# Optimization experiments

Hardware: AMD Instinct MI355X
Metric: run time of the kernel (lower is better)

Reference implementation:

```python
import jax, jax.numpy as jnp
import numpy as np
import math

B, T, D = 2, 2048, 2048
N_HEADS, N_KV, HEAD_DIM = 16, 4, 128
INTER = 8192
MAX_POS = 4096
ROPE_BASE = 10000.0
EPS = 1e-6


def _rope_tables():
    inv_freq = 1.0 / (ROPE_BASE ** (jnp.arange(0, HEAD_DIM, 2, dtype=jnp.float32) / HEAD_DIM))
    t = jnp.arange(MAX_POS, dtype=jnp.float32)
    freqs = jnp.einsum('i,j->ij', t, inv_freq)          # [MAX_POS, HEAD_DIM//2]
    emb = jnp.concatenate([freqs, freqs], axis=-1)      # [MAX_POS, HEAD_DIM]
    return jnp.cos(emb), jnp.sin(emb)


def _apply_rope(x, cos, sin):
    # x: [B,H,T,Dh]; cos/sin: [B,T,Dh] (gathered by position_ids)
    c = cos[:, None, :, :]
    s = sin[:, None, :, :]
    x1 = x[..., ::2]
    x2 = x[..., 1::2]
    x_rot = jnp.stack([-x2, x1], axis=-1).reshape(x.shape)  # interleave(-x2, x1)
    return x * c + x_rot * s


def _rms_norm(x, w):
    var = jnp.mean(x * x, axis=-1, keepdims=True)
    return w * (x * jax.lax.rsqrt(var + EPS))


def setup_inputs() -> dict:
    key = jax.random.key(0)
    ks = jax.random.split(key, 10)
    s = 0.02
    hidden_states = jax.random.normal(ks[0], (B, T, D), dtype=jnp.float32)
    # additive causal mask
    causal = jnp.tril(jnp.ones((T, T), dtype=bool))
    attention_mask = jnp.where(causal, 0.0, -1e9).astype(jnp.float32)[None, None]
    position_ids = jnp.arange(B * T).reshape(B, T)  # values < MAX_POS
    return {
        'hidden_states': hidden_states,
        'attention_mask': attention_mask,
        'position_ids': position_ids,
        'attn_norm_w': jnp.ones((D,), jnp.float32),
        'mlp_norm_w': jnp.ones((D,), jnp.float32),
        'wq': jax.random.normal(ks[1], (D, N_HEADS * HEAD_DIM), jnp.float32) * s,
        'wk': jax.random.normal(ks[2], (D, N_KV * HEAD_DIM), jnp.float32) * s,
        'wv': jax.random.normal(ks[3], (D, N_KV * HEAD_DIM), jnp.float32) * s,
        'wo': jax.random.normal(ks[4], (N_HEADS * HEAD_DIM, D), jnp.float32) * s,
        'gate_w': jax.random.normal(ks[5], (D, D), jnp.float32) * s,
        'gate_b': jnp.zeros((D,), jnp.float32),
        'fc1_w': jax.random.normal(ks[6], (D, INTER), jnp.float32) * s,
        'fc2_w': jax.random.normal(ks[7], (INTER, D), jnp.float32) * s,
    }


def reference(hidden_states, attention_mask, position_ids, attn_norm_w, mlp_norm_w,
              wq, wk, wv, wo, gate_w, gate_b, fc1_w, fc2_w):
    b, t, _ = hidden_states.shape
    residual = hidden_states
    h = _rms_norm(hidden_states, attn_norm_w)

    # elementwise sigmoid output gate: [B,T,D] -> [B,H,T,Dh]
    gate = jax.nn.sigmoid(h @ gate_w + gate_b)
    gate = gate.reshape(b, t, N_HEADS, HEAD_DIM).transpose(0, 2, 1, 3)

    q = (h @ wq).reshape(b, t, N_HEADS, HEAD_DIM).transpose(0, 2, 1, 3)
    k = (h @ wk).reshape(b, t, N_KV, HEAD_DIM).transpose(0, 2, 1, 3)
    v = (h @ wv).reshape(b, t, N_KV, HEAD_DIM).transpose(0, 2, 1, 3)

    cos_t, sin_t = _rope_tables()
    cos = cos_t[position_ids]  # [B,T,Dh]
    sin = sin_t[position_ids]
    q = _apply_rope(q, cos, sin)
    k = _apply_rope(k, cos, sin)

    n_rep = N_HEADS // N_KV
    k = jnp.repeat(k, n_rep, axis=1)  # GQA expand to [B,H,T,Dh]
    v = jnp.repeat(v, n_rep, axis=1)

    scores = jnp.einsum('bhqd,bhkd->bhqk', q, k) / math.sqrt(HEAD_DIM)
    scores = scores + attention_mask
    attn = jax.nn.softmax(scores, axis=-1)
    out = jnp.einsum('bhqk,bhkd->bhqd', attn, v) * gate
    out = out.transpose(0, 2, 1, 3).reshape(b, t, N_HEADS * HEAD_DIM) @ wo

    h = residual + out
    residual = h
    h2 = _rms_norm(h, mlp_norm_w)
    mlp_out = jax.nn.silu(h2 @ fc1_w) @ fc2_w
    return residual + mlp_out
```

## Files before the change

### kernel.cpp

```cpp
#include <hip/hip_runtime.h>
#include <hip/hip_bf16.h>
#include <cstdint>
#include <cstddef>

#define BB 2
#define TT 2048
#define DD 2048
#define NH 16
#define NKV 4
#define HD 128
#define NI 8192
#define MM (BB*TT)

typedef __bf16 bf16x8 __attribute__((ext_vector_type(8)));
typedef float  f32x4  __attribute__((ext_vector_type(4)));

__device__ __forceinline__ void gload_lds16(const void* g, void* l) {
  __builtin_amdgcn_global_load_lds((__attribute__((address_space(1))) void*)g,
                                   (__attribute__((address_space(3))) void*)l,
                                   16, 0, 0);
}

__device__ __forceinline__ int xcd_swizzle(int wg, int nwg) {
  int xcd = wg & 7;
  int l = wg >> 3;
  int q = nwg >> 3, r = nwg & 7;
  return (xcd < r ? xcd * (q + 1) : r * (q + 1) + (xcd - r) * q) + l;
}

__global__ __launch_bounds__(128) void rope_tables_k(float* __restrict__ cosT,
                                                     float* __restrict__ sinT) {
  int pos = blockIdx.x;
  int d = threadIdx.x;
  int f = d & 63;
  float inv = powf(10000.0f, -((float)(2 * f)) / 128.0f);
  float ang = inv * (float)pos;
  cosT[pos * 128 + d] = cosf(ang);
  sinT[pos * 128 + d] = sinf(ang);
}

template <typename TIN>
__global__ __launch_bounds__(256) void transpose_to_bf16_k(const TIN* __restrict__ in,
                                                           __bf16* __restrict__ out,
                                                           int R, int C) {
  __shared__ float t[32][33];
  int c0 = blockIdx.x * 32, r0 = blockIdx.y * 32;
  int tx = threadIdx.x & 31;
  int ty = threadIdx.x >> 5;
#pragma unroll
  for (int i = 0; i < 4; i++) {
    int r = ty + i * 8;
    t[r][tx] = (float)in[(size_t)(r0 + r) * C + c0 + tx];
  }
  __syncthreads();
#pragma unroll
  for (int i = 0; i < 4; i++) {
    int r = ty + i * 8;
    out[(size_t)(c0 + r) * R + r0 + tx] = (__bf16)t[tx][r];
  }
}

__global__ __launch_bounds__(256) void rmsnorm_k(const float* __restrict__ x,
                                                 const float* __restrict__ w,
                                                 __bf16* __restrict__ out) {
  int row = blockIdx.x;
  const float* xr = x + (size_t)row * DD;
  int t = threadIdx.x;
  float4 a = ((const float4*)xr)[2 * t];
  float4 b = ((const float4*)xr)[2 * t + 1];
  float ss = a.x * a.x + a.y * a.y + a.z * a.z + a.w * a.w +
             b.x * b.x + b.y * b.y + b.z * b.z + b.w * b.w;
#pragma unroll
  for (int off = 32; off; off >>= 1) ss += __shfl_xor(ss, off, 64);
  __shared__ float red[4];
  if ((t & 63) == 0) red[t >> 6] = ss;
  __syncthreads();
  float tot = red[0] + red[1] + red[2] + red[3];
  float rs = rsqrtf(tot * (1.0f / DD) + 1e-6f);
  const float4 w1 = ((const float4*)w)[2 * t];
  const float4 w2 = ((const float4*)w)[2 * t + 1];
  bf16x8 ov;
  ov[0] = (__bf16)(a.x * rs * w1.x);
  ov[1] = (__bf16)(a.y * rs * w1.y);
  ov[2] = (__bf16)(a.z * rs * w1.z);
  ov[3] = (__bf16)(a.w * rs * w1.w);
  ov[4] = (__bf16)(b.x * rs * w2.x);
  ov[5] = (__bf16)(b.y * rs * w2.y);
  ov[6] = (__bf16)(b.z * rs * w2.z);
  ov[7] = (__bf16)(b.w * rs * w2.w);
  *(bf16x8*)(out + (size_t)row * DD + t * 8) = ov;
}

enum { G_QG = 0, G_RES = 1, G_SILU = 2, G_PART = 3 };

template <int EPI>
__global__ __launch_bounds__(512) void gemm256_k(
    const __bf16* __restrict__ A, const __bf16* __restrict__ Bt,
    __bf16* __restrict__ outB, float* __restrict__ outF,
    __bf16* __restrict__ outQ, __bf16* __restrict__ outG,
    const float* __restrict__ bias, const float* __restrict__ residual,
    const float* __restrict__ cosT, const float* __restrict__ sinT,
    const int* __restrict__ posids, int N, int K, int ldk, float oscale) {
  __shared__ __align__(16) __bf16 Ab[3][256 * 32];
  __shared__ __align__(16) __bf16 Bb[3][256 * 32];
  const int tid = threadIdx.x;
  const int lane = tid & 63;
  const int wid = tid >> 6;
  const int wr = wid >> 2;
  const int wc = wid & 3;
  const int fr = lane & 15;
  const int fg = lane >> 4;

  const int nwg = gridDim.x * gridDim.y;
  int wg = xcd_swizzle(blockIdx.y * gridDim.x + blockIdx.x, nwg);
  const int bx = wg % gridDim.x, by = wg / gridDim.x;
  const int m0 = by * 256;
  const int n0 = bx * 256;
  const int kz = blockIdx.z;
  const int kBase = kz * K;

  const int srow0 = wid * 32 + (lane >> 2);
  const int scol = (((lane & 3) ^ ((lane >> 3) & 3)) << 3);
  const __bf16* aS0 = A + (size_t)(m0 + srow0) * ldk + kBase + scol;
  const __bf16* aS1 = aS0 + (size_t)16 * ldk;
  const __bf16* bS0 = Bt + (size_t)(n0 + srow0) * ldk + kBase + scol;
  const __bf16* bS1 = bS0 + (size_t)16 * ldk;
  const int e0 = (wid * 2) * 512;
  const int e1 = (wid * 2 + 1) * 512;

  const int nt = K / 32;

#define STAGE_A(kt, s)                          \
  {                                             \
    const int k0_ = (kt) * 32;                  \
    gload_lds16(aS0 + k0_, &Ab[(s)][e0]);       \
    gload_lds16(aS1 + k0_, &Ab[(s)][e1]);       \
  }
#define STAGE_B(kt, s)                          \
  {                                             \
    const int k0_ = (kt) * 32;                  \
    gload_lds16(bS0 + k0_, &Bb[(s)][e0]);       \
    gload_lds16(bS1 + k0_, &Bb[(s)][e1]);       \
  }

  STAGE_A(0, 0);
  STAGE_B(0, 0);
  STAGE_A(1, 1);
  STAGE_B(1, 1);
  asm volatile("s_waitcnt vmcnt(4)" ::: "memory");
  __builtin_amdgcn_s_barrier();

  f32x4 acc[8][4];
#pragma unroll
  for (int i = 0; i < 8; i++)
#pragma unroll
    for (int j = 0; j < 4; j++) acc[i][j] = (f32x4){0.f, 0.f, 0.f, 0.f};

  const int asl = (fg ^ ((fr >> 1) & 3)) * 8;

  for (int t = 0; t < nt; ++t) {
    const int s = t % 3;
    const int sn = (t + 2) % 3;
    bf16x8 af[4], bfr[4];
#pragma unroll
    for (int mi = 0; mi < 4; mi++)
      af[mi] = *(const bf16x8*)&Ab[s][(wr * 128 + mi * 16 + fr) * 32 + asl];
#pragma unroll
    for (int ni = 0; ni < 4; ni++)
      bfr[ni] = *(const bf16x8*)&Bb[s][(wc * 64 + ni * 16 + fr) * 32 + asl];
    if (t + 2 < nt) STAGE_A(t + 2, sn);
    __builtin_amdgcn_s_barrier();
    asm volatile("s_waitcnt lgkmcnt(0)" ::: "memory");
    __builtin_amdgcn_sched_barrier(0);
    __builtin_amdgcn_s_setprio(1);
#pragma unroll
    for (int mi = 0; mi < 4; mi++)
#pragma unroll
      for (int ni = 0; ni < 4; ni++)
        acc[mi][ni] =
            __builtin_amdgcn_mfma_f32_16x16x32_bf16(af[mi], bfr[ni], acc[mi][ni], 0, 0, 0);
    __builtin_amdgcn_s_setprio(0);
    __builtin_amdgcn_s_barrier();
    bf16x8 af2[4];
#pragma unroll
    for (int mi = 0; mi < 4; mi++)
      af2[mi] = *(const bf16x8*)&Ab[s][(wr * 128 + (mi + 4) * 16 + fr) * 32 + asl];
    if (t + 2 < nt) {
      STAGE_B(t + 2, sn);
      asm volatile("s_waitcnt vmcnt(4)" ::: "memory");
    } else {
      asm volatile("s_waitcnt vmcnt(0)" ::: "memory");
    }
    __builtin_amdgcn_s_barrier();
    asm volatile("s_waitcnt lgkmcnt(0)" ::: "memory");
    __builtin_amdgcn_sched_barrier(0);
    __builtin_amdgcn_s_setprio(1);
#pragma unroll
    for (int mi = 0; mi < 4; mi++)
#pragma unroll
      for (int ni = 0; ni < 4; ni++)
        acc[mi + 4][ni] =
            __builtin_amdgcn_mfma_f32_16x16x32_bf16(af2[mi], bfr[ni], acc[mi + 4][ni], 0, 0, 0);
    __builtin_amdgcn_s_setprio(0);
    __builtin_amdgcn_s_barrier();
  }
#undef STAGE_A
#undef STAGE_B

#pragma unroll
  for (int mi = 0; mi < 8; mi++) {
    const int row = m0 + wr * 128 + mi * 16 + fg * 4;
#pragma unroll
    for (int ni = 0; ni < 4; ni++) {
      const int col = n0 + wc * 64 + ni * 16 + fr;
#pragma unroll
      for (int j = 0; j < 4; j++) {
        float v = acc[mi][ni][j];
        const int r = row + j;
        if constexpr (EPI == G_QG) {
          float vp = __shfl_xor(v, 1, 64);
          if (n0 < 2048) {
            int pos = posids[r];
            int d = col & 127;
            float c = cosT[pos * 128 + d], sn2 = sinT[pos * 128 + d];
            float o = (col & 1) ? (v * c + vp * sn2) : (v * c - vp * sn2);
            outQ[(size_t)r * 2048 + col] = (__bf16)(o * oscale);
          } else {
            float xx = v + bias[col - 2048];
            outG[(size_t)r * 2048 + (col - 2048)] = (__bf16)(1.0f / (1.0f + expf(-xx)));
          }
        } else if constexpr (EPI == G_RES) {
          outF[(size_t)r * N + col] = v + residual[(size_t)r * N + col];
        } else if constexpr (EPI == G_SILU) {
          outB[(size_t)r * N + col] = (__bf16)(v / (1.0f + expf(-v)));
        } else {
          outB[(size_t)(kz * MM + r) * N + col] = (__bf16)v;
        }
      }
    }
  }
}

__global__ __launch_bounds__(256) void combine_k(const __bf16* __restrict__ parts,
                                                 const float* __restrict__ res,
                                                 float* __restrict__ out) {
  size_t i = ((size_t)blockIdx.x * 256 + threadIdx.x) * 8;
  bf16x8 p0 = *(const bf16x8*)&parts[i];
  bf16x8 p1 = *(const bf16x8*)&parts[(size_t)MM * 2048 + i];
  float4 a = *(const float4*)&res[i];
  float4 b = *(const float4*)&res[i + 4];
  float4 o0, o1;
  o0.x = (float)p0[0] + (float)p1[0] + a.x;
  o0.y = (float)p0[1] + (float)p1[1] + a.y;
  o0.z = (float)p0[2] + (float)p1[2] + a.z;
  o0.w = (float)p0[3] + (float)p1[3] + a.w;
  o1.x = (float)p0[4] + (float)p1[4] + b.x;
  o1.y = (float)p0[5] + (float)p1[5] + b.y;
  o1.z = (float)p0[6] + (float)p1[6] + b.z;
  o1.w = (float)p0[7] + (float)p1[7] + b.w;
  *(float4*)&out[i] = o0;
  *(float4*)&out[i + 4] = o1;
}

__global__ __launch_bounds__(256) void gemm_kv_k(
    const __bf16* __restrict__ A, const __bf16* __restrict__ Bt,
    __bf16* __restrict__ kOut, __bf16* __restrict__ vOut,
    const float* __restrict__ cosT, const float* __restrict__ sinT,
    const int* __restrict__ posids, int K) {
  __shared__ __align__(16) __bf16 As[128 * 32];
  __shared__ __align__(16) __bf16 Bs[128 * 32];
  const int tid = threadIdx.x;
  const int lane = tid & 63;
  const int w = tid >> 6;
  const int wm = w >> 1, wn = w & 1;

  const int nwg = gridDim.x * gridDim.y;
  int wg = xcd_swizzle(blockIdx.y * gridDim.x + blockIdx.x, nwg);
  const int bx = wg % gridDim.x, by = wg / gridDim.x;
  const int m0 = by * 128;
  const int n0 = bx * 128;

  const int lr = lane >> 2;
  const int lc = (lane & 3) * 8;
  const __bf16* aSrc = A + (size_t)(m0 + 32 * w + lr) * K + lc;
  const __bf16* bSrc = Bt + (size_t)(n0 + 32 * w + lr) * K + lc;
  __bf16* aDst = &As[w * 1024];
  __bf16* bDst = &Bs[w * 1024];

  f32x4 acc[4][4];
#pragma unroll
  for (int i = 0; i < 4; i++)
#pragma unroll
    for (int j = 0; j < 4; j++) acc[i][j] = (f32x4){0.f, 0.f, 0.f, 0.f};

  const int fr = lane & 15;
  const int fc = (lane >> 4) * 8;

  for (int k0 = 0; k0 < K; k0 += 32) {
    __syncthreads();
    gload_lds16(aSrc + k0, aDst);
    gload_lds16(aSrc + k0 + (size_t)16 * K, aDst + 512);
    gload_lds16(bSrc + k0, bDst);
    gload_lds16(bSrc + k0 + (size_t)16 * K, bDst + 512);
    asm volatile("s_waitcnt vmcnt(0)" ::: "memory");
    __syncthreads();

    bf16x8 af[4], bfg[4];
#pragma unroll
    for (int i = 0; i < 4; i++)
      af[i] = *(const bf16x8*)&As[(wm * 64 + i * 16 + fr) * 32 + fc];
#pragma unroll
    for (int i = 0; i < 4; i++)
      bfg[i] = *(const bf16x8*)&Bs[(wn * 64 + i * 16 + fr) * 32 + fc];
#pragma unroll
    for (int mi = 0; mi < 4; mi++)
#pragma unroll
      for (int ni = 0; ni < 4; ni++)
        acc[mi][ni] =
            __builtin_amdgcn_mfma_f32_16x16x32_bf16(af[mi], bfg[ni], acc[mi][ni], 0, 0, 0);
  }

  const int fg = lane >> 4;
#pragma unroll
  for (int mi = 0; mi < 4; mi++) {
#pragma unroll
    for (int ni = 0; ni < 4; ni++) {
#pragma unroll
      for (int j = 0; j < 4; j++) {
        int row = m0 + wm * 64 + mi * 16 + fg * 4 + j;
        int col = n0 + wn * 64 + ni * 16 + fr;
        float v = acc[mi][ni][j];
        float vp = __shfl_xor(v, 1, 64);
        if (col < 512) {
          int pos = posids[row];
          int d = col & 127;
          float c = cosT[pos * 128 + d];
          float s = sinT[pos * 128 + d];
          float o = (col & 1) ? (v * c + vp * s) : (v * c - vp * s);
          kOut[(size_t)row * 512 + col] = (__bf16)o;
        } else {
          vOut[(size_t)row * 512 + (col - 512)] = (__bf16)v;
        }
      }
    }
  }
}

__global__ __launch_bounds__(256) void attn_k(const __bf16* __restrict__ Q,
                                              const __bf16* __restrict__ Kb,
                                              const __bf16* __restrict__ Vt,
                                              const __bf16* __restrict__ Gate,
                                              __bf16* __restrict__ Out) {
  __shared__ __align__(16) __bf16 Ks[2][64 * 128];
  __shared__ __align__(16) __bf16 Vs[2][128 * 64];
  __shared__ __align__(16) __bf16 Ps[4][16 * 64];
  const int tid = threadIdx.x;
  const int lane = tid & 63;
  const int w = tid >> 6;
  const int fr = lane & 15;
  const int fg = lane >> 4;

  const int nwg = gridDim.x * gridDim.y;
  int wg = xcd_swizzle(blockIdx.y * gridDim.x + blockIdx.x, nwg);
  const int qb = wg % gridDim.x;
  const int bh = wg / gridDim.x;
  const int q0 = qb * 64;
  const int b = bh >> 4, h = bh & 15;
  const int g = h >> 2;

  const size_t qrow = (size_t)(b * TT + q0 + w * 16 + fr);
  bf16x8 qf[4];
#pragma unroll
  for (int kt = 0; kt < 4; kt++)
    qf[kt] = *(const bf16x8*)&Q[qrow * 2048 + h * 128 + kt * 32 + fg * 8];

  const __bf16* kPtr[4];
  const __bf16* vPtr[4];
#pragma unroll
  for (int i = 0; i < 4; i++) {
    int krow = w * 16 + i * 4 + (lane >> 4);
    int kcol8 = (lane & 15) ^ (krow & 15);
    kPtr[i] = Kb + (size_t)(b * TT + krow) * 512 + g * 128 + kcol8 * 8;
    int dloc = w * 32 + i * 8 + (lane >> 3);
    int kv8 = (lane & 7) ^ (dloc & 7);
    vPtr[i] = Vt + (size_t)(g * 128 + dloc) * (size_t)MM + b * TT + kv8 * 8;
  }

  f32x4 o[8];
#pragma unroll
  for (int i = 0; i < 8; i++) o[i] = (f32x4){0.f, 0.f, 0.f, 0.f};
  float mrow[4] = {-3e38f, -3e38f, -3e38f, -3e38f};
  float lrow[4] = {0.f, 0.f, 0.f, 0.f};

  const int nsteps = qb + 1;

#pragma unroll
  for (int i = 0; i < 4; i++) {
    gload_lds16(kPtr[i], &Ks[0][w * 2048 + i * 512]);
    gload_lds16(vPtr[i], &Vs[0][w * 2048 + i * 512]);
  }
  __syncthreads();

  for (int t = 0; t < nsteps; t++) {
    const int cur = t & 1;
    const int kb = t * 64;
    if (t + 1 < nsteps) {
      const int nb = kb + 64;
#pragma unroll
      for (int i = 0; i < 4; i++) {
        gload_lds16(kPtr[i] + (size_t)nb * 512, &Ks[cur ^ 1][w * 2048 + i * 512]);
        gload_lds16(vPtr[i] + nb, &Vs[cur ^ 1][w * 2048 + i * 512]);
      }
    }

    f32x4 s[4];
#pragma unroll
    for (int nc = 0; nc < 4; nc++) s[nc] = (f32x4){0.f, 0.f, 0.f, 0.f};
#pragma unroll
    for (int nc = 0; nc < 4; nc++)
#pragma unroll
      for (int kt = 0; kt < 4; kt++) {
        bf16x8 kf = *(const bf16x8*)&Ks[cur][(nc * 16 + fr) * 128 + (((kt * 4 + fg) ^ fr) << 3)];
        s[nc] = __builtin_amdgcn_mfma_f32_16x16x32_bf16(qf[kt], kf, s[nc], 0, 0, 0);
      }

    float alpha[4];
#pragma unroll
    for (int j = 0; j < 4; j++) {
      const int qr = q0 + w * 16 + fg * 4 + j;
      float pv[4];
#pragma unroll
      for (int nc = 0; nc < 4; nc++) {
        int kc = kb + nc * 16 + fr;
        float val = s[nc][j];
        if (kc > qr) val = -1e9f;
        pv[nc] = val;
      }
      float tmx = fmaxf(fmaxf(pv[0], pv[1]), fmaxf(pv[2], pv[3]));
      tmx = fmaxf(tmx, __shfl_xor(tmx, 1, 64));
      tmx = fmaxf(tmx, __shfl_xor(tmx, 2, 64));
      tmx = fmaxf(tmx, __shfl_xor(tmx, 4, 64));
      tmx = fmaxf(tmx, __shfl_xor(tmx, 8, 64));
      float mnew = fmaxf(mrow[j], tmx);
      alpha[j] = __expf(mrow[j] - mnew);
      mrow[j] = mnew;
      float rsum = 0.f;
      const int q = fg * 4 + j;
#pragma unroll
      for (int nc = 0; nc < 4; nc++) {
        float e = __expf(pv[nc] - mnew);
        rsum += e;
        Ps[w][q * 64 + (((nc * 2 + (fr >> 3)) ^ (q & 7)) << 3) + (fr & 7)] = (__bf16)e;
      }
      rsum += __shfl_xor(rsum, 1, 64);
      rsum += __shfl_xor(rsum, 2, 64);
      rsum += __shfl_xor(rsum, 4, 64);
      rsum += __shfl_xor(rsum, 8, 64);
      lrow[j] = lrow[j] * alpha[j] + rsum;
    }
#pragma unroll
    for (int nd = 0; nd < 8; nd++)
#pragma unroll
      for (int j = 0; j < 4; j++) o[nd][j] *= alpha[j];

    bf16x8 pa[2];
#pragma unroll
    for (int sl = 0; sl < 2; sl++)
      pa[sl] = *(const bf16x8*)&Ps[w][fr * 64 + (((sl * 4 + fg) ^ (fr & 7)) << 3)];
#pragma unroll
    for (int nd = 0; nd < 8; nd++)
#pragma unroll
      for (int sl = 0; sl < 2; sl++) {
        bf16x8 vf =
            *(const bf16x8*)&Vs[cur][(nd * 16 + fr) * 64 + (((sl * 4 + fg) ^ (fr & 7)) << 3)];
        o[nd] = __builtin_amdgcn_mfma_f32_16x16x32_bf16(pa[sl], vf, o[nd], 0, 0, 0);
      }
    __syncthreads();
  }

  float invl[4];
#pragma unroll
  for (int j = 0; j < 4; j++) invl[j] = 1.0f / lrow[j];
#pragma unroll
  for (int nd = 0; nd < 8; nd++) {
#pragma unroll
    for (int j = 0; j < 4; j++) {
      int row = q0 + w * 16 + fg * 4 + j;
      int d = nd * 16 + fr;
      size_t idx = (size_t)(b * TT + row) * 2048 + h * 128 + d;
      float val = o[nd][j] * invl[j] * (float)Gate[idx];
      Out[idx] = (__bf16)val;
    }
  }
}

extern "C" void kernel_launch(void* const* d_in, const int* in_sizes, int n_in,
                              void* d_out, int out_size, void* d_ws, size_t ws_size,
                              hipStream_t stream) {
  const float* hidden = (const float*)d_in[0];
  const int* posids = (const int*)d_in[2];
  const float* attn_w = (const float*)d_in[3];
  const float* mlp_w = (const float*)d_in[4];
  const float* wq = (const float*)d_in[5];
  const float* wk = (const float*)d_in[6];
  const float* wv = (const float*)d_in[7];
  const float* wo = (const float*)d_in[8];
  const float* gw = (const float*)d_in[9];
  const float* gb = (const float*)d_in[10];
  const float* f1 = (const float*)d_in[11];
  const float* f2 = (const float*)d_in[12];

  char* p = (char*)d_ws;
  auto alloc = [&](size_t n) {
    char* r = p;
    p += (n + 255) & ~(size_t)255;
    return r;
  };
  __bf16* wqg_t = (__bf16*)alloc((size_t)4096 * 2048 * 2);
  __bf16* wkv_t = (__bf16*)alloc((size_t)1024 * 2048 * 2);
  __bf16* wo_t = (__bf16*)alloc((size_t)2048 * 2048 * 2);
  __bf16* f1_t = (__bf16*)alloc((size_t)NI * 2048 * 2);
  __bf16* f2_t = (__bf16*)alloc((size_t)2048 * NI * 2);
  __bf16* h_bf = (__bf16*)alloc((size_t)MM * DD * 2);
  float* h1 = (float*)alloc((size_t)MM * 2048 * 4);

  char* regionA = alloc((size_t)64 * 1024 * 1024);
  __bf16* q_bf = (__bf16*)(regionA);
  __bf16* gate_bf = (__bf16*)(regionA + (size_t)16 * 1024 * 1024);
  __bf16* attn_g = (__bf16*)(regionA + (size_t)32 * 1024 * 1024);
  __bf16* k_bf = (__bf16*)(regionA + (size_t)48 * 1024 * 1024);
  __bf16* v_bf = (__bf16*)(regionA + (size_t)52 * 1024 * 1024);
  __bf16* v_t = (__bf16*)(regionA + (size_t)56 * 1024 * 1024);
  float* cosT = (float*)(regionA + (size_t)60 * 1024 * 1024);
  float* sinT = (float*)(regionA + (size_t)62 * 1024 * 1024);
  __bf16* mlp1 = (__bf16*)(regionA);
  __bf16* parts_wo = (__bf16*)(regionA);
  __bf16* parts_fc2 = (__bf16*)f1_t;

  rope_tables_k<<<4096, 128, 0, stream>>>(cosT, sinT);

  transpose_to_bf16_k<float><<<dim3(64, 64), 256, 0, stream>>>(wq, wqg_t, 2048, 2048);
  transpose_to_bf16_k<float><<<dim3(64, 64), 256, 0, stream>>>(gw, wqg_t + (size_t)2048 * 2048, 2048, 2048);
  transpose_to_bf16_k<float><<<dim3(16, 64), 256, 0, stream>>>(wk, wkv_t, 2048, 512);
  transpose_to_bf16_k<float><<<dim3(16, 64), 256, 0, stream>>>(wv, wkv_t + (size_t)512 * 2048, 2048, 512);
  transpose_to_bf16_k<float><<<dim3(64, 64), 256, 0, stream>>>(wo, wo_t, 2048, 2048);
  transpose_to_bf16_k<float><<<dim3(256, 64), 256, 0, stream>>>(f1, f1_t, 2048, NI);
  transpose_to_bf16_k<float><<<dim3(64, 256), 256, 0, stream>>>(f2, f2_t, NI, 2048);

  rmsnorm_k<<<MM, 256, 0, stream>>>(hidden, attn_w, h_bf);

  const float qsc = 0.08838834764831845f;
  gemm256_k<G_QG><<<dim3(16, 16), 512, 0, stream>>>(
      h_bf, wqg_t, nullptr, nullptr, q_bf, gate_bf, gb, nullptr, cosT, sinT, posids,
      4096, 2048, 2048, qsc);
  gemm_kv_k<<<dim3(8, 32), 256, 0, stream>>>(h_bf, wkv_t, k_bf, v_bf, cosT, sinT, posids, 2048);

  transpose_to_bf16_k<__bf16><<<dim3(16, 128), 256, 0, stream>>>(v_bf, v_t, MM, 512);

  attn_k<<<dim3(32, 32), 256, 0, stream>>>(q_bf, k_bf, v_t, gate_bf, attn_g);

  gemm256_k<G_PART><<<dim3(8, 16, 2), 512, 0, stream>>>(
      attn_g, wo_t, parts_wo, nullptr, nullptr, nullptr, nullptr, nullptr, nullptr, nullptr,
      nullptr, 2048, 1024, 2048, 1.0f);
  combine_k<<<4096, 256, 0, stream>>>(parts_wo, hidden, h1);

  rmsnorm_k<<<MM, 256, 0, stream>>>(h1, mlp_w, h_bf);

  gemm256_k<G_SILU><<<dim3(32, 16), 512, 0, stream>>>(
      h_bf, f1_t, mlp1, nullptr, nullptr, nullptr, nullptr, nullptr, nullptr, nullptr, nullptr,
      NI, 2048, 2048, 1.0f);

  gemm256_k<G_PART><<<dim3(8, 16, 2), 512, 0, stream>>>(
      mlp1, f2_t, parts_fc2, nullptr, nullptr, nullptr, nullptr, nullptr, nullptr, nullptr,
      nullptr, 2048, 4096, NI, 1.0f);

  combine_k<<<4096, 256, 0, stream>>>(parts_fc2, h1, (float*)d_out);
}
```

Baseline: 792.8 us.

## Deepen GEMM LDS pipeline to four stages with unrolled k-loop and tile grouping

```diff
diff --git a/kernel.cpp b/kernel.cpp
--- a/kernel.cpp
+++ b/kernel.cpp
@@ -101,8 +101,8 @@
     const float* __restrict__ bias, const float* __restrict__ residual,
     const float* __restrict__ cosT, const float* __restrict__ sinT,
     const int* __restrict__ posids, int N, int K, int ldk, float oscale) {
-  __shared__ __align__(16) __bf16 Ab[3][256 * 32];
-  __shared__ __align__(16) __bf16 Bb[3][256 * 32];
+  __shared__ __align__(16) __bf16 Ab[4][256 * 32];
+  __shared__ __align__(16) __bf16 Bb[4][256 * 32];
   const int tid = threadIdx.x;
   const int lane = tid & 63;
   const int wid = tid >> 6;
@@ -111,9 +111,13 @@
   const int fr = lane & 15;
   const int fg = lane >> 4;
 
-  const int nwg = gridDim.x * gridDim.y;
-  int wg = xcd_swizzle(blockIdx.y * gridDim.x + blockIdx.x, nwg);
-  const int bx = wg % gridDim.x, by = wg / gridDim.x;
+  const int gx = gridDim.x, gy = gridDim.y;
+  const int nwg = gx * gy;
+  int wg = xcd_swizzle(blockIdx.y * gx + blockIdx.x, nwg);
+  const int scW = gy * 8;
+  const int sc = wg / scW, rem = wg % scW;
+  const int by = rem >> 3;
+  const int bx = sc * 8 + (rem & 7);
   const int m0 = by * 256;
   const int n0 = bx * 256;
   const int kz = blockIdx.z;
@@ -125,29 +129,27 @@
   const __bf16* aS1 = aS0 + (size_t)16 * ldk;
   const __bf16* bS0 = Bt + (size_t)(n0 + srow0) * ldk + kBase + scol;
   const __bf16* bS1 = bS0 + (size_t)16 * ldk;
-  const int e0 = (wid * 2) * 512;
-  const int e1 = (wid * 2 + 1) * 512;
+  const int e0 = wid * 1024;
+  const int e1 = wid * 1024 + 512;
 
   const int nt = K / 32;
 
-#define STAGE_A(kt, s)                          \
-  {                                             \
-    const int k0_ = (kt) * 32;                  \
-    gload_lds16(aS0 + k0_, &Ab[(s)][e0]);       \
-    gload_lds16(aS1 + k0_, &Ab[(s)][e1]);       \
-  }
-#define STAGE_B(kt, s)                          \
-  {                                             \
-    const int k0_ = (kt) * 32;                  \
-    gload_lds16(bS0 + k0_, &Bb[(s)][e0]);       \
-    gload_lds16(bS1 + k0_, &Bb[(s)][e1]);       \
-  }
-
-  STAGE_A(0, 0);
-  STAGE_B(0, 0);
-  STAGE_A(1, 1);
-  STAGE_B(1, 1);
-  asm volatile("s_waitcnt vmcnt(4)" ::: "memory");
+#define STG_A(T, S)                                        \
+  {                                                        \
+    const size_t ko = (size_t)(T) * 32;                    \
+    gload_lds16(aS0 + ko, &Ab[(S)][e0]);                   \
+    gload_lds16(aS1 + ko, &Ab[(S)][e1]);                   \
+  }
+#define STG_B(T, S)                                        \
+  {                                                        \
+    const size_t ko = (size_t)(T) * 32;                    \
+    gload_lds16(bS0 + ko, &Bb[(S)][e0]);                   \
+    gload_lds16(bS1 + ko, &Bb[(S)][e1]);                   \
+  }
+  STG_A(0, 0); STG_B(0, 0);
+  STG_A(1, 1); STG_B(1, 1);
+  STG_A(2, 2); STG_B(2, 2);
+  asm volatile("s_waitcnt vmcnt(8)" ::: "memory");
   __builtin_amdgcn_s_barrier();
 
   f32x4 acc[8][4];
@@ -158,54 +160,57 @@
 
   const int asl = (fg ^ ((fr >> 1) & 3)) * 8;
 
-  for (int t = 0; t < nt; ++t) {
-    const int s = t % 3;
-    const int sn = (t + 2) % 3;
-    bf16x8 af[4], bfr[4];
-#pragma unroll
-    for (int mi = 0; mi < 4; mi++)
-      af[mi] = *(const bf16x8*)&Ab[s][(wr * 128 + mi * 16 + fr) * 32 + asl];
-#pragma unroll
-    for (int ni = 0; ni < 4; ni++)
-      bfr[ni] = *(const bf16x8*)&Bb[s][(wc * 64 + ni * 16 + fr) * 32 + asl];
-    if (t + 2 < nt) STAGE_A(t + 2, sn);
-    __builtin_amdgcn_s_barrier();
-    asm volatile("s_waitcnt lgkmcnt(0)" ::: "memory");
-    __builtin_amdgcn_sched_barrier(0);
-    __builtin_amdgcn_s_setprio(1);
-#pragma unroll
-    for (int mi = 0; mi < 4; mi++)
-#pragma unroll
-      for (int ni = 0; ni < 4; ni++)
-        acc[mi][ni] =
-            __builtin_amdgcn_mfma_f32_16x16x32_bf16(af[mi], bfr[ni], acc[mi][ni], 0, 0, 0);
-    __builtin_amdgcn_s_setprio(0);
-    __builtin_amdgcn_s_barrier();
-    bf16x8 af2[4];
-#pragma unroll
-    for (int mi = 0; mi < 4; mi++)
-      af2[mi] = *(const bf16x8*)&Ab[s][(wr * 128 + (mi + 4) * 16 + fr) * 32 + asl];
-    if (t + 2 < nt) {
-      STAGE_B(t + 2, sn);
-      asm volatile("s_waitcnt vmcnt(4)" ::: "memory");
-    } else {
-      asm volatile("s_waitcnt vmcnt(0)" ::: "memory");
-    }
-    __builtin_amdgcn_s_barrier();
-    asm volatile("s_waitcnt lgkmcnt(0)" ::: "memory");
-    __builtin_amdgcn_sched_barrier(0);
-    __builtin_amdgcn_s_setprio(1);
-#pragma unroll
-    for (int mi = 0; mi < 4; mi++)
-#pragma unroll
-      for (int ni = 0; ni < 4; ni++)
-        acc[mi + 4][ni] =
-            __builtin_amdgcn_mfma_f32_16x16x32_bf16(af2[mi], bfr[ni], acc[mi + 4][ni], 0, 0, 0);
-    __builtin_amdgcn_s_setprio(0);
-    __builtin_amdgcn_s_barrier();
-  }
-#undef STAGE_A
-#undef STAGE_B
+#define KSTEP(T, SUB, DOSTAGE, VM)                                                    \
+  {                                                                                   \
+    bf16x8 af[4], bfr[4], af2[4];                                                     \
+    _Pragma("unroll") for (int mi = 0; mi < 4; mi++)                                  \
+      af[mi] = *(const bf16x8*)&Ab[SUB][(wr * 128 + mi * 16 + fr) * 32 + asl];        \
+    _Pragma("unroll") for (int ni = 0; ni < 4; ni++)                                  \
+      bfr[ni] = *(const bf16x8*)&Bb[SUB][(wc * 64 + ni * 16 + fr) * 32 + asl];        \
+    if (DOSTAGE) STG_A((T) + 3, ((SUB) + 3) & 3);                                     \
+    __builtin_amdgcn_s_barrier();                                                     \
+    asm volatile("s_waitcnt lgkmcnt(0)" ::: "memory");                                \
+    __builtin_amdgcn_sched_barrier(0);                                                \
+    __builtin_amdgcn_s_setprio(1);                                                    \
+    _Pragma("unroll") for (int mi = 0; mi < 4; mi++)                                  \
+      _Pragma("unroll") for (int ni = 0; ni < 4; ni++)                                \
+        acc[mi][ni] =                                                                 \
+            __builtin_amdgcn_mfma_f32_16x16x32_bf16(af[mi], bfr[ni], acc[mi][ni], 0, 0, 0); \
+    __builtin_amdgcn_s_setprio(0);                                                    \
+    __builtin_amdgcn_s_barrier();                                                     \
+    _Pragma("unroll") for (int mi = 0; mi < 4; mi++)                                  \
+      af2[mi] = *(const bf16x8*)&Ab[SUB][(wr * 128 + (mi + 4) * 16 + fr) * 32 + asl]; \
+    if (DOSTAGE) STG_B((T) + 3, ((SUB) + 3) & 3);                                     \
+    __builtin_amdgcn_s_barrier();                                                     \
+    asm volatile("s_waitcnt lgkmcnt(0)" ::: "memory");                                \
+    __builtin_amdgcn_sched_barrier(0);                                                \
+    __builtin_amdgcn_s_setprio(1);                                                    \
+    _Pragma("unroll") for (int mi = 0; mi < 4; mi++)                                  \
+      _Pragma("unroll") for (int ni = 0; ni < 4; ni++)                                \
+        acc[mi + 4][ni] =                                                             \
+            __builtin_amdgcn_mfma_f32_16x16x32_bf16(af2[mi], bfr[ni], acc[mi + 4][ni], 0, 0, 0); \
+    __builtin_amdgcn_s_setprio(0);                                                    \
+    asm volatile("s_waitcnt vmcnt(" #VM ")" ::: "memory");                            \
+    __builtin_amdgcn_s_barrier();                                                     \
+  }
+
+  for (int it = 0; it < nt / 4 - 1; ++it) {
+    const int t0 = it * 4;
+    KSTEP(t0 + 0, 0, 1, 8);
+    KSTEP(t0 + 1, 1, 1, 8);
+    KSTEP(t0 + 2, 2, 1, 8);
+    KSTEP(t0 + 3, 3, 1, 8);
+  }
+  {
+    const int t0 = nt - 4;
+    KSTEP(t0 + 0, 0, 1, 8);
+    KSTEP(t0 + 1, 1, 0, 4);
+    KSTEP(t0 + 2, 2, 0, 0);
+    KSTEP(t0 + 3, 3, 0, 0);
+  }
+#undef KSTEP
+#undef STG_A
+#undef STG_B
 
 #pragma unroll
   for (int mi = 0; mi < 8; mi++) {
```

New measurement: 805.6 us. No clear change (+1.6%).

## Split GEMM main loop into four phases and fuse residual combine with RMSNorm

Applied to the files above, without the earlier changes.

```diff
diff --git a/kernel.cpp b/kernel.cpp
--- a/kernel.cpp
+++ b/kernel.cpp
@@ -130,23 +130,13 @@
 
   const int nt = K / 32;
 
-#define STAGE_A(kt, s)                          \
-  {                                             \
-    const int k0_ = (kt) * 32;                  \
-    gload_lds16(aS0 + k0_, &Ab[(s)][e0]);       \
-    gload_lds16(aS1 + k0_, &Ab[(s)][e1]);       \
-  }
-#define STAGE_B(kt, s)                          \
-  {                                             \
-    const int k0_ = (kt) * 32;                  \
-    gload_lds16(bS0 + k0_, &Bb[(s)][e0]);       \
-    gload_lds16(bS1 + k0_, &Bb[(s)][e1]);       \
-  }
-
-  STAGE_A(0, 0);
-  STAGE_B(0, 0);
-  STAGE_A(1, 1);
-  STAGE_B(1, 1);
+#define STG_A0(kt, s) gload_lds16(aS0 + (kt) * 32, &Ab[(s)][e0]);
+#define STG_A1(kt, s) gload_lds16(aS1 + (kt) * 32, &Ab[(s)][e1]);
+#define STG_B0(kt, s) gload_lds16(bS0 + (kt) * 32, &Bb[(s)][e0]);
+#define STG_B1(kt, s) gload_lds16(bS1 + (kt) * 32, &Bb[(s)][e1]);
+
+  STG_A0(0, 0); STG_A1(0, 0); STG_B0(0, 0); STG_B1(0, 0);
+  STG_A0(1, 1); STG_A1(1, 1); STG_B0(1, 1); STG_B1(1, 1);
   asm volatile("s_waitcnt vmcnt(4)" ::: "memory");
   __builtin_amdgcn_s_barrier();
 
@@ -161,51 +151,67 @@
   for (int t = 0; t < nt; ++t) {
     const int s = t % 3;
     const int sn = (t + 2) % 3;
-    bf16x8 af[4], bfr[4];
-#pragma unroll
-    for (int mi = 0; mi < 4; mi++)
-      af[mi] = *(const bf16x8*)&Ab[s][(wr * 128 + mi * 16 + fr) * 32 + asl];
-#pragma unroll
-    for (int ni = 0; ni < 4; ni++)
-      bfr[ni] = *(const bf16x8*)&Bb[s][(wc * 64 + ni * 16 + fr) * 32 + asl];
-    if (t + 2 < nt) STAGE_A(t + 2, sn);
-    __builtin_amdgcn_s_barrier();
-    asm volatile("s_waitcnt lgkmcnt(0)" ::: "memory");
-    __builtin_amdgcn_sched_barrier(0);
-    __builtin_amdgcn_s_setprio(1);
-#pragma unroll
-    for (int mi = 0; mi < 4; mi++)
+    const bool dostage = (t + 2 < nt);
+    bf16x8 bfr[4];
+
+    {
+      bf16x8 af[2];
+#pragma unroll
+      for (int mi = 0; mi < 2; mi++)
+        af[mi] = *(const bf16x8*)&Ab[s][(wr * 128 + mi * 16 + fr) * 32 + asl];
 #pragma unroll
       for (int ni = 0; ni < 4; ni++)
-        acc[mi][ni] =
-            __builtin_amdgcn_mfma_f32_16x16x32_bf16(af[mi], bfr[ni], acc[mi][ni], 0, 0, 0);
-    __builtin_amdgcn_s_setprio(0);
-    __builtin_amdgcn_s_barrier();
-    bf16x8 af2[4];
-#pragma unroll
-    for (int mi = 0; mi < 4; mi++)
-      af2[mi] = *(const bf16x8*)&Ab[s][(wr * 128 + (mi + 4) * 16 + fr) * 32 + asl];
-    if (t + 2 < nt) {
-      STAGE_B(t + 2, sn);
-      asm volatile("s_waitcnt vmcnt(4)" ::: "memory");
-    } else {
-      asm volatile("s_waitcnt vmcnt(0)" ::: "memory");
+        bfr[ni] = *(const bf16x8*)&Bb[s][(wc * 64 + ni * 16 + fr) * 32 + asl];
+      if (dostage) STG_A0(t + 2, sn);
+      __builtin_amdgcn_s_barrier();
+      asm volatile("s_waitcnt lgkmcnt(0)" ::: "memory");
+      __builtin_amdgcn_sched_barrier(0);
+      __builtin_amdgcn_s_setprio(1);
+#pragma unroll
+      for (int mi = 0; mi < 2; mi++)
+#pragma unroll
+        for (int ni = 0; ni < 4; ni++)
+          acc[mi][ni] =
+              __builtin_amdgcn_mfma_f32_16x16x32_bf16(af[mi], bfr[ni], acc[mi][ni], 0, 0, 0);
+      __builtin_amdgcn_s_setprio(0);
+      __builtin_amdgcn_s_barrier();
     }
-    __builtin_amdgcn_s_barrier();
-    asm volatile("s_waitcnt lgkmcnt(0)" ::: "memory");
-    __builtin_amdgcn_sched_barrier(0);
-    __builtin_amdgcn_s_setprio(1);
-#pragma unroll
-    for (int mi = 0; mi < 4; mi++)
-#pragma unroll
-      for (int ni = 0; ni < 4; ni++)
-        acc[mi + 4][ni] =
-            __builtin_amdgcn_mfma_f32_16x16x32_bf16(af2[mi], bfr[ni], acc[mi + 4][ni], 0, 0, 0);
-    __builtin_amdgcn_s_setprio(0);
-    __builtin_amdgcn_s_barrier();
-  }
-#undef STAGE_A
-#undef STAGE_B
+#pragma unroll
+    for (int ph = 1; ph < 4; ph++) {
+      bf16x8 af[2];
+#pragma unroll
+      for (int mi = 0; mi < 2; mi++)
+        af[mi] = *(const bf16x8*)&Ab[s][(wr * 128 + (ph * 2 + mi) * 16 + fr) * 32 + asl];
+      if (dostage) {
+        if (ph == 1) { STG_A1(t + 2, sn); }
+        else if (ph == 2) { STG_B0(t + 2, sn); }
+        else { STG_B1(t + 2, sn); }
+      }
+      __builtin_amdgcn_s_barrier();
+      asm volatile("s_waitcnt lgkmcnt(0)" ::: "memory");
+      __builtin_amdgcn_sched_barrier(0);
+      __builtin_amdgcn_s_setprio(1);
+#pragma unroll
+      for (int mi = 0; mi < 2; mi++)
+#pragma unroll
+        for (int ni = 0; ni < 4; ni++)
+          acc[ph * 2 + mi][ni] = __builtin_amdgcn_mfma_f32_16x16x32_bf16(
+              af[mi], bfr[ni], acc[ph * 2 + mi][ni], 0, 0, 0);
+      __builtin_amdgcn_s_setprio(0);
+      if (ph == 3) {
+        if (dostage) {
+          asm volatile("s_waitcnt vmcnt(4)" ::: "memory");
+        } else {
+          asm volatile("s_waitcnt vmcnt(0)" ::: "memory");
+        }
+      }
+      __builtin_amdgcn_s_barrier();
+    }
+  }
+#undef STG_A0
+#undef STG_A1
+#undef STG_B0
+#undef STG_B1
 
 #pragma unroll
   for (int mi = 0; mi < 8; mi++) {
@@ -262,6 +268,55 @@
   *(float4*)&out[i + 4] = o1;
 }
 
+__global__ __launch_bounds__(256) void combine_rms_k(const __bf16* __restrict__ parts,
+                                                     const float* __restrict__ res,
+                                                     const float* __restrict__ w,
+                                                     float* __restrict__ h1,
+                                                     __bf16* __restrict__ h2) {
+  const int row = blockIdx.x;
+  const int t = threadIdx.x;
+  const size_t i = (size_t)row * 2048 + t * 8;
+  bf16x8 p0 = *(const bf16x8*)&parts[i];
+  bf16x8 p1 = *(const bf16x8*)&parts[(size_t)MM * 2048 + i];
+  float4 a = *(const float4*)&res[i];
+  float4 b = *(const float4*)&res[i + 4];
+  float v[8];
+  v[0] = (float)p0[0] + (float)p1[0] + a.x;
+  v[1] = (float)p0[1] + (float)p1[1] + a.y;
+  v[2] = (float)p0[2] + (float)p1[2] + a.z;
+  v[3] = (float)p0[3] + (float)p1[3] + a.w;
+  v[4] = (float)p0[4] + (float)p1[4] + b.x;
+  v[5] = (float)p0[5] + (float)p1[5] + b.y;
+  v[6] = (float)p0[6] + (float)p1[6] + b.z;
+  v[7] = (float)p0[7] + (float)p1[7] + b.w;
+  float4 o0 = {v[0], v[1], v[2], v[3]};
+  float4 o1 = {v[4], v[5], v[6], v[7]};
+  *(float4*)&h1[i] = o0;
+  *(float4*)&h1[i + 4] = o1;
+  float ss = 0.f;
+#pragma unroll
+  for (int k = 0; k < 8; k++) ss += v[k] * v[k];
+#pragma unroll
+  for (int off = 32; off; off >>= 1) ss += __shfl_xor(ss, off, 64);
+  __shared__ float red[4];
+  if ((t & 63) == 0) red[t >> 6] = ss;
+  __syncthreads();
+  float tot = red[0] + red[1] + red[2] + red[3];
+  float rs = rsqrtf(tot * (1.0f / DD) + 1e-6f);
+  const float4 w1 = ((const float4*)w)[2 * t];
+  const float4 w2 = ((const float4*)w)[2 * t + 1];
+  bf16x8 ov;
+  ov[0] = (__bf16)(v[0] * rs * w1.x);
+  ov[1] = (__bf16)(v[1] * rs * w1.y);
+  ov[2] = (__bf16)(v[2] * rs * w1.z);
+  ov[3] = (__bf16)(v[3] * rs * w1.w);
+  ov[4] = (__bf16)(v[4] * rs * w2.x);
+  ov[5] = (__bf16)(v[5] * rs * w2.y);
+  ov[6] = (__bf16)(v[6] * rs * w2.z);
+  ov[7] = (__bf16)(v[7] * rs * w2.w);
+  *(bf16x8*)(h2 + i) = ov;
+}
+
 __global__ __launch_bounds__(256) void gemm_kv_k(
     const __bf16* __restrict__ A, const __bf16* __restrict__ Bt,
     __bf16* __restrict__ kOut, __bf16* __restrict__ vOut,
@@ -562,9 +617,7 @@
   gemm256_k<G_PART><<<dim3(8, 16, 2), 512, 0, stream>>>(
       attn_g, wo_t, parts_wo, nullptr, nullptr, nullptr, nullptr, nullptr, nullptr, nullptr,
       nullptr, 2048, 1024, 2048, 1.0f);
-  combine_k<<<4096, 256, 0, stream>>>(parts_wo, hidden, h1);
-
-  rmsnorm_k<<<MM, 256, 0, stream>>>(h1, mlp_w, h_bf);
+  combine_rms_k<<<MM, 256, 0, stream>>>(parts_wo, hidden, mlp_w, h1, h_bf);
 
   gemm256_k<G_SILU><<<dim3(32, 16), 512, 0, stream>>>(
       h_bf, f1_t, mlp1, nullptr, nullptr, nullptr, nullptr, nullptr, nullptr, nullptr, nullptr,
```

Measured after the change: 880.2 us. 11.0% more time.

## Fuse residual combine with MLP RMSNorm and use BK=64 pipelined GEMM for fc1

Applied to the files above, without the earlier changes.

```diff
diff --git a/kernel.cpp b/kernel.cpp
--- a/kernel.cpp
+++ b/kernel.cpp
@@ -241,6 +241,174 @@
   }
 }
 
+template <int EPI>
+__global__ __launch_bounds__(512, 1) void gemm256x64_k(
+    const __bf16* __restrict__ A, const __bf16* __restrict__ Bt,
+    __bf16* __restrict__ outB, float* __restrict__ outF,
+    __bf16* __restrict__ outQ, __bf16* __restrict__ outG,
+    const float* __restrict__ bias, const float* __restrict__ residual,
+    const float* __restrict__ cosT, const float* __restrict__ sinT,
+    const int* __restrict__ posids, int N, int K, int ldk, float oscale) {
+  __shared__ __align__(16) __bf16 Ab[2][256 * 64];
+  __shared__ __align__(16) __bf16 Bb[2][256 * 64];
+  const int tid = threadIdx.x;
+  const int lane = tid & 63;
+  const int wid = tid >> 6;
+  const int wr = wid >> 2;
+  const int wc = wid & 3;
+  const int fr = lane & 15;
+  const int fg = lane >> 4;
+
+  const int nwg = gridDim.x * gridDim.y;
+  int wg = xcd_swizzle(blockIdx.y * gridDim.x + blockIdx.x, nwg);
+  const int bx = wg % gridDim.x, by = wg / gridDim.x;
+  const int m0 = by * 256;
+  const int n0 = bx * 256;
+  const int kz = blockIdx.z;
+  const int kBase = kz * K;
+
+  const int rofs = lane >> 3;
+  const int swz = ((lane & 7) ^ rofs) * 8;
+  const int gA0 = ((wid & 4) << 5) + ((wid & 3) << 4);
+  const int gB0 = ((wid >> 1) << 6) + ((wid & 1) << 4);
+  const __bf16* aSrcB = A + (size_t)(m0 + rofs) * ldk + kBase + swz;
+  const __bf16* bSrcB = Bt + (size_t)(n0 + rofs) * ldk + kBase + swz;
+
+  const int nt = K / 64;
+
+#define STGA64(buf, h, T)                                                            \
+  {                                                                                  \
+    const int g0_ = gA0 + (h) * 64;                                                  \
+    gload_lds16(aSrcB + (size_t)g0_ * ldk + (size_t)(T) * 64, &Ab[buf][g0_ * 64]);   \
+    gload_lds16(aSrcB + (size_t)(g0_ + 8) * ldk + (size_t)(T) * 64,                  \
+                &Ab[buf][(g0_ + 8) * 64]);                                           \
+  }
+#define STGB64(buf, h, T)                                                            \
+  {                                                                                  \
+    const int g0_ = gB0 + (h) * 32;                                                  \
+    gload_lds16(bSrcB + (size_t)g0_ * ldk + (size_t)(T) * 64, &Bb[buf][g0_ * 64]);   \
+    gload_lds16(bSrcB + (size_t)(g0_ + 8) * ldk + (size_t)(T) * 64,                  \
+                &Bb[buf][(g0_ + 8) * 64]);                                           \
+  }
+#define RD64_A(dst, buf, mh)                                                           \
+  _Pragma("unroll") for (int mt = 0; mt < 4; mt++)                                     \
+  _Pragma("unroll") for (int kk = 0; kk < 2; kk++)                                     \
+      dst[mt][kk] = *(const bf16x8*)&Ab[buf][(wr * 128 + (mh) * 64 + mt * 16 + fr) * 64 + \
+                                             (((kk * 4 + fg) ^ (fr & 7)) << 3)];
+#define RD64_B(dst, buf, nh)                                                           \
+  _Pragma("unroll") for (int nt2 = 0; nt2 < 2; nt2++)                                  \
+  _Pragma("unroll") for (int kk = 0; kk < 2; kk++)                                     \
+      dst[nt2][kk] = *(const bf16x8*)&Bb[buf][(wc * 64 + (nh) * 32 + nt2 * 16 + fr) * 64 + \
+                                              (((kk * 4 + fg) ^ (fr & 7)) << 3)];
+#define MFMA64(a, b, MH, NHh)                                                          \
+  _Pragma("unroll") for (int mt = 0; mt < 4; mt++)                                     \
+  _Pragma("unroll") for (int nt2 = 0; nt2 < 2; nt2++)                                  \
+  _Pragma("unroll") for (int kk = 0; kk < 2; kk++)                                     \
+      acc[(MH) * 4 + mt][(NHh) * 2 + nt2] = __builtin_amdgcn_mfma_f32_16x16x32_bf16(   \
+          a[mt][kk], b[nt2][kk], acc[(MH) * 4 + mt][(NHh) * 2 + nt2], 0, 0, 0);
+#define PH_SYNC                                           \
+  __builtin_amdgcn_s_barrier();                           \
+  asm volatile("s_waitcnt lgkmcnt(0)" ::: "memory");      \
+  __builtin_amdgcn_sched_barrier(0);                      \
+  __builtin_amdgcn_s_setprio(1);
+#define PH_END                                            \
+  __builtin_amdgcn_s_setprio(0);                          \
+  __builtin_amdgcn_s_barrier();
+
+#define TILE64(T, CUR, OTH, S0, S123, VMSTR)              \
+  {                                                       \
+    bf16x8 a0[4][2], a1[4][2], b0[2][2], b1[2][2];        \
+    RD64_A(a0, CUR, 0);                                   \
+    RD64_B(b0, CUR, 0);                                   \
+    if (S0) STGB64(OTH, 0, (T) + 1);                      \
+    PH_SYNC;                                              \
+    MFMA64(a0, b0, 0, 0);                                 \
+    PH_END;                                               \
+    RD64_B(b1, CUR, 1);                                   \
+    if (S123) STGA64(CUR, 0, (T) + 2);                    \
+    PH_SYNC;                                              \
+    MFMA64(a0, b1, 0, 1);                                 \
+    PH_END;                                               \
+    RD64_A(a1, CUR, 1);                                   \
+    if (S123) STGB64(CUR, 1, (T) + 2);                    \
+    PH_SYNC;                                              \
+    MFMA64(a1, b1, 1, 1);                                 \
+    PH_END;                                               \
+    RD64_B(b0, CUR, 0);                                   \
+    if (S123) STGA64(CUR, 1, (T) + 2);                    \
+    __builtin_amdgcn_s_barrier();                         \
+    asm volatile("s_waitcnt lgkmcnt(0)" ::: "memory");    \
+    __builtin_amdgcn_sched_barrier(0);                    \
+    __builtin_amdgcn_s_setprio(1);                        \
+    MFMA64(a1, b0, 1, 0);                                 \
+    __builtin_amdgcn_s_setprio(0);                        \
+    asm volatile("s_waitcnt " VMSTR ::: "memory");        \
+    __builtin_amdgcn_s_barrier();                         \
+  }
+
+  f32x4 acc[8][4];
+#pragma unroll
+  for (int i = 0; i < 8; i++)
+#pragma unroll
+    for (int j = 0; j < 4; j++) acc[i][j] = (f32x4){0.f, 0.f, 0.f, 0.f};
+
+  STGB64(0, 0, 0); STGA64(0, 0, 0); STGB64(0, 1, 0); STGA64(0, 1, 0);
+  STGA64(1, 0, 1); STGB64(1, 1, 1); STGA64(1, 1, 1);
+  asm volatile("s_waitcnt vmcnt(6)" ::: "memory");
+  __builtin_amdgcn_s_barrier();
+
+  for (int t = 0; t < nt; t += 2) {
+    if (t + 2 < nt) {
+      TILE64(t, 0, 1, true, true, "vmcnt(6)");
+      TILE64(t + 1, 1, 0, true, true, "vmcnt(6)");
+    } else {
+      TILE64(t, 0, 1, true, false, "vmcnt(0)");
+      TILE64(t + 1, 1, 0, false, false, "vmcnt(0)");
+    }
+  }
+#undef TILE64
+#undef PH_SYNC
+#undef PH_END
+#undef MFMA64
+#undef RD64_A
+#undef RD64_B
+#undef STGA64
+#undef STGB64
+
+#pragma unroll
+  for (int mi = 0; mi < 8; mi++) {
+    const int row = m0 + wr * 128 + mi * 16 + fg * 4;
+#pragma unroll
+    for (int ni = 0; ni < 4; ni++) {
+      const int col = n0 + wc * 64 + ni * 16 + fr;
+#pragma unroll
+      for (int j = 0; j < 4; j++) {
+        float v = acc[mi][ni][j];
+        const int r = row + j;
+        if constexpr (EPI == G_QG) {
+          float vp = __shfl_xor(v, 1, 64);
+          if (n0 < 2048) {
+            int pos = posids[r];
+            int d = col & 127;
+            float c = cosT[pos * 128 + d], sn2 = sinT[pos * 128 + d];
+            float o = (col & 1) ? (v * c + vp * sn2) : (v * c - vp * sn2);
+            outQ[(size_t)r * 2048 + col] = (__bf16)(o * oscale);
+          } else {
+            float xx = v + bias[col - 2048];
+            outG[(size_t)r * 2048 + (col - 2048)] = (__bf16)(1.0f / (1.0f + expf(-xx)));
+          }
+        } else if constexpr (EPI == G_RES) {
+          outF[(size_t)r * N + col] = v + residual[(size_t)r * N + col];
+        } else if constexpr (EPI == G_SILU) {
+          outB[(size_t)r * N + col] = (__bf16)(v / (1.0f + expf(-v)));
+        } else {
+          outB[(size_t)(kz * MM + r) * N + col] = (__bf16)v;
+        }
+      }
+    }
+  }
+}
+
 __global__ __launch_bounds__(256) void combine_k(const __bf16* __restrict__ parts,
                                                  const float* __restrict__ res,
                                                  float* __restrict__ out) {
@@ -262,6 +430,55 @@
   *(float4*)&out[i + 4] = o1;
 }
 
+__global__ __launch_bounds__(256) void combine_rms_k(const __bf16* __restrict__ parts,
+                                                     const float* __restrict__ res,
+                                                     const float* __restrict__ w,
+                                                     float* __restrict__ h1,
+                                                     __bf16* __restrict__ h2) {
+  const int row = blockIdx.x;
+  const int t = threadIdx.x;
+  const size_t i = (size_t)row * 2048 + t * 8;
+  bf16x8 p0 = *(const bf16x8*)&parts[i];
+  bf16x8 p1 = *(const bf16x8*)&parts[(size_t)MM * 2048 + i];
+  float4 a = *(const float4*)&res[i];
+  float4 b = *(const float4*)&res[i + 4];
+  float v[8];
+  v[0] = (float)p0[0] + (float)p1[0] + a.x;
+  v[1] = (float)p0[1] + (float)p1[1] + a.y;
+  v[2] = (float)p0[2] + (float)p1[2] + a.z;
+  v[3] = (float)p0[3] + (float)p1[3] + a.w;
+  v[4] = (float)p0[4] + (float)p1[4] + b.x;
+  v[5] = (float)p0[5] + (float)p1[5] + b.y;
+  v[6] = (float)p0[6] + (float)p1[6] + b.z;
+  v[7] = (float)p0[7] + (float)p1[7] + b.w;
+  float4 o0 = {v[0], v[1], v[2], v[3]};
+  float4 o1 = {v[4], v[5], v[6], v[7]};
+  *(float4*)&h1[i] = o0;
+  *(float4*)&h1[i + 4] = o1;
+  float ss = 0.f;
+#pragma unroll
+  for (int k = 0; k < 8; k++) ss += v[k] * v[k];
+#pragma unroll
+  for (int off = 32; off; off >>= 1) ss += __shfl_xor(ss, off, 64);
+  __shared__ float red[4];
+  if ((t & 63) == 0) red[t >> 6] = ss;
+  __syncthreads();
+  float tot = red[0] + red[1] + red[2] + red[3];
+  float rs = rsqrtf(tot * (1.0f / DD) + 1e-6f);
+  const float4 w1 = ((const float4*)w)[2 * t];
+  const float4 w2 = ((const float4*)w)[2 * t + 1];
+  bf16x8 ov;
+  ov[0] = (__bf16)(v[0] * rs * w1.x);
+  ov[1] = (__bf16)(v[1] * rs * w1.y);
+  ov[2] = (__bf16)(v[2] * rs * w1.z);
+  ov[3] = (__bf16)(v[3] * rs * w1.w);
+  ov[4] = (__bf16)(v[4] * rs * w2.x);
+  ov[5] = (__bf16)(v[5] * rs * w2.y);
+  ov[6] = (__bf16)(v[6] * rs * w2.z);
+  ov[7] = (__bf16)(v[7] * rs * w2.w);
+  *(bf16x8*)(h2 + i) = ov;
+}
+
 __global__ __launch_bounds__(256) void gemm_kv_k(
     const __bf16* __restrict__ A, const __bf16* __restrict__ Bt,
     __bf16* __restrict__ kOut, __bf16* __restrict__ vOut,
@@ -562,11 +779,9 @@
   gemm256_k<G_PART><<<dim3(8, 16, 2), 512, 0, stream>>>(
       attn_g, wo_t, parts_wo, nullptr, nullptr, nullptr, nullptr, nullptr, nullptr, nullptr,
       nullptr, 2048, 1024, 2048, 1.0f);
-  combine_k<<<4096, 256, 0, stream>>>(parts_wo, hidden, h1);
-
-  rmsnorm_k<<<MM, 256, 0, stream>>>(h1, mlp_w, h_bf);
-
-  gemm256_k<G_SILU><<<dim3(32, 16), 512, 0, stream>>>(
+  combine_rms_k<<<MM, 256, 0, stream>>>(parts_wo, hidden, mlp_w, h1, h_bf);
+
+  gemm256x64_k<G_SILU><<<dim3(32, 16), 512, 0, stream>>>(
       h_bf, f1_t, mlp1, nullptr, nullptr, nullptr, nullptr, nullptr, nullptr, nullptr, nullptr,
       NI, 2048, 2048, 1.0f);
 
```

Result: slower. 1.342 ms (+69.2%).
